# Kernel tuning notes

Measured on AMD Instinct MI355X. Metric: run time of the kernel, lower is better.

The kernel has to match this reference:

```python
import jax, jax.numpy as jnp
import numpy as np

EPS = 1e-7            # keras.backend.epsilon()
NEG = -1e30           # log-space 'zero' (avoid -inf for NaN-free grads)
SUB_SAMPLE = (2, 2)   # encoder conv subsampling factors (non-tensor forward arg)


def setup_inputs() -> dict:
    key = jax.random.key(0)
    k1, k2, k3, k4 = jax.random.split(key, 4)
    B, T, C, L = 128, 2000, 128, 200
    logits = jax.random.normal(k1, (B, T, C), jnp.float32)
    y_pred = jax.nn.softmax(logits, axis=-1)  # ctc_batch_cost expects probabilities
    labels = jax.random.randint(k2, (B, L), 0, C - 1, jnp.int32)  # never the blank (C-1)
    # raw frame counts; after two /2 subsamplings -> in [1000, 2000] <= T
    feat_lens = jax.random.randint(k3, (B,), 4000, 8000, jnp.int32)
    label_lens = jax.random.randint(k4, (B,), 50, L + 1, jnp.int32)
    return {"y_pred": y_pred, "labels": labels, "feat_lens": feat_lens, "label_lens": label_lens}


def _ctc_batch_cost(y_pred, labels, feat_lens, label_lens):
    """Faithful reimplementation of keras.backend.ctc_batch_cost (blank = C-1),
    with the CTCLayer's subsampling of feat_lens applied first."""
    for sub in SUB_SAMPLE:
        if sub > 1:
            feat_lens = (feat_lens + 1) // sub
    log_probs = jnp.log(y_pred + EPS)                 # [B,T,C]
    B, T, C = y_pred.shape
    L = labels.shape[1]
    S = 2 * L + 1
    blank = C - 1

    # extended label sequence: blank, l1, blank, l2, ..., blank  -> [B,S]
    ext = jnp.full((B, S), blank, jnp.int32).at[:, 1::2].set(labels)
    # skip transition s-2 -> s allowed iff ext[s] != blank and ext[s] != ext[s-2]
    skip_ok = jnp.concatenate(
        [jnp.zeros((B, 2), bool), (ext[:, 2:] != blank) & (ext[:, 2:] != ext[:, :-2])],
        axis=1,
    )
    bidx = jnp.arange(B)
    i1 = 2 * label_lens - 1   # last non-blank state
    i2 = 2 * label_lens       # trailing blank state

    lp = jnp.swapaxes(log_probs, 0, 1)                # [T,B,C], scan over time

    emit0 = jnp.take_along_axis(lp[0], ext, axis=1)   # [B,S]
    alpha0 = (jnp.full((B, S), NEG, jnp.float32)
              .at[:, 0].set(emit0[:, 0])
              .at[:, 1].set(emit0[:, 1]))
    ll0 = jnp.logaddexp(alpha0[bidx, i1], alpha0[bidx, i2])
    final0 = jnp.where(feat_lens == 1, ll0, NEG)

    def step(carry, inp):
        alpha, final = carry
        t, lp_t = inp
        emit = jnp.take_along_axis(lp_t, ext, axis=1)              # [B,S]
        a1 = jnp.pad(alpha, ((0, 0), (1, 0)), constant_values=NEG)[:, :-1]
        a2 = jnp.pad(alpha, ((0, 0), (2, 0)), constant_values=NEG)[:, :-2]
        m = jnp.logaddexp(alpha, a1)
        m = jnp.where(skip_ok, jnp.logaddexp(m, a2), m)
        alpha = m + emit
        ll = jnp.logaddexp(alpha[bidx, i1], alpha[bidx, i2])
        final = jnp.where(t == feat_lens - 1, ll, final)           # capture at last valid frame
        return (alpha, final), None

    (_, final), _ = jax.lax.scan(step, (alpha0, final0), (jnp.arange(1, T), lp[1:]))
    return -final[:, None]                                          # [B,1] like ctc_batch_cost


def reference(y_pred, labels, feat_lens, label_lens):
    return _ctc_batch_cost(y_pred, labels, feat_lens, label_lens)
```

## Files before the change

kernel.cpp:

```cpp
#include <hip/hip_runtime.h>
#include <math.h>

#define EPSQ 1e-7f
#define TDIM 2000
#define CDIM 128
#define LDIM 200
#define SPL  7
#define SENTE (-(1 << 30))

#define RING  0
#define LABSI 16384
#define PRODF 16584
#define CONSF 16585
#define SMEMN 16592


__device__ __forceinline__ float dpp_shr_f(float x) {
    return __int_as_float(__builtin_amdgcn_update_dpp(0, __float_as_int(x), 0x138, 0xf, 0xf, true));
}
__device__ __forceinline__ int dpp_shr_i(int x) {
    return __builtin_amdgcn_update_dpp(0, x, 0x138, 0xf, 0xf, true);
}
__device__ __forceinline__ float dpp_shl_f(float x) {
    return __int_as_float(__builtin_amdgcn_update_dpp(0, __float_as_int(x), 0x130, 0xf, 0xf, true));
}
__device__ __forceinline__ int dpp_shl_i(int x) {
    return __builtin_amdgcn_update_dpp(0, x, 0x130, 0xf, 0xf, true);
}

__device__ __forceinline__ void renorm_alpha(float a[SPL], int& E, float& fprev, int lane) {
    float mx = fmaxf(fmaxf(fmaxf(a[0], a[1]), fmaxf(a[2], a[3])),
                     fmaxf(fmaxf(a[4], a[5]), a[6]));
    bool zero = (mx == 0.f);
    int e = ((__float_as_int(mx) >> 23) & 0xff) - 127;
    int S_self = zero ? SENTE : (E + e);
    int S1 = dpp_shr_i(S_self);
    if (lane == 0) S1 = SENTE;
    int S2 = dpp_shr_i(S1);
    if (lane == 0) S2 = SENTE;
    int E_new = max(S_self, S1);
    int E_prevnew = max(S1, S2);
    int dg = E - E_new;
    float g = (zero || dg < -126) ? 0.f : __int_as_float((dg + 127) << 23);
#pragma unroll
    for (int j = 0; j < SPL; ++j) a[j] *= g;
    E = E_new;
    int df = E_prevnew - E_new;
    bool fz = (E_prevnew <= SENTE / 2) || (df < -126);
    if (df > 126) df = 126;
    fprev = fz ? 0.f : __int_as_float((df + 127) << 23);
}

__device__ __forceinline__ void renorm_beta(float b[SPL], int& E, float& fnext, int lane) {
    float mx = fmaxf(fmaxf(fmaxf(b[0], b[1]), fmaxf(b[2], b[3])),
                     fmaxf(fmaxf(b[4], b[5]), b[6]));
    bool zero = (mx == 0.f);
    int e = ((__float_as_int(mx) >> 23) & 0xff) - 127;
    int S_self = zero ? SENTE : (E + e);
    int S1 = dpp_shl_i(S_self);
    if (lane == 63) S1 = SENTE;
    int S2 = dpp_shl_i(S1);
    if (lane == 63) S2 = SENTE;
    int E_new = max(S_self, S1);
    int E_nextnew = max(S1, S2);
    int dg = E - E_new;
    float g = (zero || dg < -126) ? 0.f : __int_as_float((dg + 127) << 23);
#pragma unroll
    for (int j = 0; j < SPL; ++j) b[j] *= g;
    E = E_new;
    int df = E_nextnew - E_new;
    bool fz = (E_nextnew <= SENTE / 2) || (df < -126);
    if (df > 126) df = 126;
    fnext = fz ? 0.f : __int_as_float((df + 127) << 23);
}

#define A_STEP(TOFF) do {                                                     \
    float p6 = dpp_shr_f(a[6]) * fprev;                                       \
    float p5 = dpp_shr_f(a[5]) * fprev;                                       \
    float n0 = fmaf(skipf[0], p5,   a[0] + p6)   * q[(1+(TOFF))&3][0];        \
    float n1 = fmaf(skipf[1], p6,   a[1] + a[0]) * q[(1+(TOFF))&3][1];        \
    float n2 = fmaf(skipf[2], a[0], a[2] + a[1]) * q[(1+(TOFF))&3][2];        \
    float n3 = fmaf(skipf[3], a[1], a[3] + a[2]) * q[(1+(TOFF))&3][3];        \
    float n4 = fmaf(skipf[4], a[2], a[4] + a[3]) * q[(1+(TOFF))&3][4];        \
    float n5 = fmaf(skipf[5], a[3], a[5] + a[4]) * q[(1+(TOFF))&3][5];        \
    float n6 = fmaf(skipf[6], a[4], a[6] + a[5]) * q[(1+(TOFF))&3][6];        \
    a[0]=n0; a[1]=n1; a[2]=n2; a[3]=n3; a[4]=n4; a[5]=n5; a[6]=n6;            \
    if (t + (TOFF) == m) {                                                    \
        _Pragma("unroll")                                                     \
        for (int j = 0; j < SPL; ++j) ac[j] = a[j];                           \
        Eac = E;                                                              \
    }                                                                         \
    {   const int rr = ((t + (TOFF) + 3) & 127) << 7;                         \
        _Pragma("unroll")                                                     \
        for (int j = 0; j < SPL; ++j)                                         \
            q[(TOFF)&3][j] = ring[rr + cls[j]];                               \
    }                                                                         \
} while (0);

#define B_STEP(SOFF) do {                                                     \
    float c0 = bb[0]*q[(SOFF)&3][0], c1 = bb[1]*q[(SOFF)&3][1];               \
    float c2 = bb[2]*q[(SOFF)&3][2], c3 = bb[3]*q[(SOFF)&3][3];               \
    float c4 = bb[4]*q[(SOFF)&3][4], c5 = bb[5]*q[(SOFF)&3][5];               \
    float c6 = bb[6]*q[(SOFF)&3][6];                                          \
    float cn0 = dpp_shl_f(c0) * fnext;                                        \
    float cn1 = dpp_shl_f(c1) * fnext;                                        \
    bb[0] = fmaf(skb[0], c2, c0 + c1);                                        \
    bb[1] = fmaf(skb[1], c3, c1 + c2);                                        \
    bb[2] = fmaf(skb[2], c4, c2 + c3);                                        \
    bb[3] = fmaf(skb[3], c5, c3 + c4);                                        \
    bb[4] = fmaf(skb[4], c6, c4 + c5);                                        \
    bb[5] = fmaf(skb[5], cn0, c5 + c6);                                       \
    bb[6] = fmaf(skb[6], cn1, c6 + cn0);                                      \
    if (s + (SOFF) == scap) {                                                 \
        _Pragma("unroll")                                                     \
        for (int j = 0; j < SPL; ++j) bc[j] = bb[j];                          \
        Ebc = E;                                                              \
    }                                                                         \
    {   const int rr = ((t0 - s - (SOFF) - 3) & 127) << 7;                    \
        _Pragma("unroll")                                                     \
        for (int j = 0; j < SPL; ++j)                                         \
            q[(3+(SOFF))&3][j] = ring[rr + cls[j]];                           \
    }                                                                         \
} while (0);

#define LOADG(W, G) do {                                                      \
    _Pragma("unroll")                                                         \
    for (int i_ = 0; i_ < 8; ++i_) {                                          \
        int ii_ = (G) * 8 + i_; if (ii_ > iend) ii_ = iend;                   \
        int pr_ = role ? (pbase - ii_) : ii_;                                 \
        W[i_] = rp4[pr_ * 64 + lane];                                         \
    }                                                                         \
} while (0)

#define STOREG(W, G) do {                                                     \
    _Pragma("unroll")                                                         \
    for (int i_ = 0; i_ < 8; ++i_) {                                          \
        int ii_ = (G) * 8 + i_; if (ii_ > iend) ii_ = iend;                   \
        int pr_ = role ? (pbase - ii_) : ii_;                                 \
        float4 x_ = W[i_];                                                    \
        x_.x += EPSQ; x_.y += EPSQ; x_.z += EPSQ; x_.w += EPSQ;               \
        *(float4*)&smf[RING + (pr_ & 63) * 256 + lane * 4] = x_;              \
    }                                                                         \
} while (0)

__global__ void __launch_bounds__(128, 1)
__attribute__((amdgpu_waves_per_eu(1, 1)))
ctc_kernel(const float* __restrict__ y_pred,
           const int* __restrict__ labels,
           const int* __restrict__ feat_lens,
           const int* __restrict__ label_lens,
           float* __restrict__ ws)
{
    __shared__ int smem[SMEMN];
    float* smf = (float*)smem;
    volatile int* vsm = (volatile int*)smem;

    const int bid = blockIdx.x;
    const int b = bid >> 1;
    const int role = bid & 1;
    const int tid = threadIdx.x;
    const int lane = tid & 63;
    const int wv = tid >> 6;

    int f = feat_lens[b];
    f = (f + 1) >> 1; f = (f + 1) >> 1;
    const int Tbm1 = f - 1;
    const int m = f >> 1;

    if (tid < 2) smem[PRODF + tid] = 0;
    const int* labrow = labels + b * LDIM;
    for (int i = tid; i < LDIM; i += 128) smem[LABSI + i] = labrow[i];
    __syncthreads();

    const float4* rp4 = (const float4*)(y_pred + (size_t)b * TDIM * CDIM);

    if (wv == 1) {
        int iend, pbase;
        if (role == 0) { iend = (m + 18) >> 1; pbase = 0; }
        else {
            const int pstart = Tbm1 >> 1;
            int pl = (m - 18) >> 1; if (pl < 0) pl = 0;
            iend = pstart - pl; pbase = pstart;
        }
        const int ng = (iend >> 3) + 1;
        float4 w0[8], w1[8];
        LOADG(w0, 0);
        if (ng > 1) LOADG(w1, 1);
        int g = 0;
        while (true) {
            while (vsm[CONSF] + 64 < 8 * (g + 1)) __builtin_amdgcn_s_sleep(2);
            asm volatile("" ::: "memory");
            STOREG(w0, g);
            asm volatile("s_waitcnt lgkmcnt(0)" ::: "memory");
            vsm[PRODF] = 8 * (g + 1);
            if (g + 2 < ng) LOADG(w0, g + 2);
            ++g; if (g >= ng) break;
            while (vsm[CONSF] + 64 < 8 * (g + 1)) __builtin_amdgcn_s_sleep(2);
            asm volatile("" ::: "memory");
            STOREG(w1, g);
            asm volatile("s_waitcnt lgkmcnt(0)" ::: "memory");
            vsm[PRODF] = 8 * (g + 1);
            if (g + 2 < ng) LOADG(w1, g + 2);
            ++g; if (g >= ng) break;
        }
        return;
    }

    const int llen = label_lens[b];
    const int i1 = 2 * llen - 1, i2 = 2 * llen;
    int cls[SPL]; float skipf[SPL];
    const int s0 = lane * SPL;
#pragma unroll
    for (int j = 0; j < SPL; ++j) {
        int s = s0 + j;
        int c = CDIM - 1; float sk = 0.f;
        if (s < (2 * LDIM + 1) && (s & 1)) {
            int kk = s >> 1;
            c = smem[LABSI + kk];
            if (kk >= 1 && smem[LABSI + kk] != smem[LABSI + kk - 1]) sk = 1.f;
        }
        cls[j] = c; skipf[j] = sk;
    }
    const float* ring = &smf[RING];

    if (role == 0) {
        float a[SPL], q[4][SPL], ac[SPL];
        int E = 0, Eac = 0;
        float fprev = 0.f;
#pragma unroll
        for (int j = 0; j < SPL; ++j) { a[j] = 0.f; ac[j] = 0.f; }

        while (vsm[PRODF] < 2) __builtin_amdgcn_s_sleep(1);
        asm volatile("" ::: "memory");
#pragma unroll
        for (int j = 0; j < SPL; ++j) {
            q[0][j] = ring[(0 << 7) + cls[j]];
            q[1][j] = ring[(1 << 7) + cls[j]];
            q[2][j] = ring[(2 << 7) + cls[j]];
            q[3][j] = ring[(3 << 7) + cls[j]];
        }
        if (lane == 0) { a[0] = q[0][0]; a[1] = q[0][1]; }

        int t = 1;
        while (t <= m) {
            vsm[CONSF] = (t >= 2) ? (((t - 2) >> 1) + 1) : 0;
            int need = ((t + 18) >> 1) + 1;
            while (vsm[PRODF] < need) __builtin_amdgcn_s_sleep(1);
            asm volatile("" ::: "memory");
            renorm_alpha(a, E, fprev, lane);
            A_STEP(0) A_STEP(1) A_STEP(2) A_STEP(3)
            renorm_alpha(a, E, fprev, lane);
            A_STEP(4) A_STEP(5) A_STEP(6) A_STEP(7)
            renorm_alpha(a, E, fprev, lane);
            A_STEP(8) A_STEP(9) A_STEP(10) A_STEP(11)
            renorm_alpha(a, E, fprev, lane);
            A_STEP(12) A_STEP(13) A_STEP(14) A_STEP(15)
            t += 16;
        }
        vsm[CONSF] = 1 << 28;
        asm volatile("" ::: "memory");
        float* wsb = ws + (size_t)b * 1024;
#pragma unroll
        for (int j = 0; j < SPL; ++j) wsb[lane * SPL + j] = ac[j];
        ((int*)wsb)[448 + lane] = Eac;
    } else {
        float bb[SPL], q[4][SPL], bc[SPL];
        int E = 0, Ebc = 0;
        float fnext = 0.f;
#pragma unroll
        for (int j = 0; j < SPL; ++j) {
            int s = s0 + j;
            bb[j] = (s == i1 || s == i2) ? 1.f : 0.f;
            bc[j] = 0.f;
        }
        float skb[SPL];
#pragma unroll
        for (int j = 0; j < 5; ++j) skb[j] = skipf[j + 2];
        skb[5] = (lane == 63) ? 0.f : __shfl_down(skipf[0], 1, 64);
        skb[6] = (lane == 63) ? 0.f : __shfl_down(skipf[1], 1, 64);

        const int t0 = Tbm1;
        const int nb = t0 - m;
        const int scap = nb - 1;
        const int pstart = t0 >> 1;

        while (vsm[PRODF] < 2) __builtin_amdgcn_s_sleep(1);
        asm volatile("" ::: "memory");
#pragma unroll
        for (int j = 0; j < SPL; ++j) {
            q[0][j] = ring[((t0 & 127) << 7) + cls[j]];
            q[1][j] = ring[(((t0 - 1) & 127) << 7) + cls[j]];
            q[2][j] = ring[(((t0 - 2) & 127) << 7) + cls[j]];
            q[3][j] = 0.f;
        }

        int s = 0;
        while (s < nb) {
            int tcur = t0 - s;
            vsm[CONSF] = pstart - ((tcur + 2) >> 1) + 1;
            int need = pstart - ((tcur - 18) >> 1) + 1;
            while (vsm[PRODF] < need) __builtin_amdgcn_s_sleep(1);
            asm volatile("" ::: "memory");
            renorm_beta(bb, E, fnext, lane);
            B_STEP(0) B_STEP(1) B_STEP(2) B_STEP(3)
            renorm_beta(bb, E, fnext, lane);
            B_STEP(4) B_STEP(5) B_STEP(6) B_STEP(7)
            renorm_beta(bb, E, fnext, lane);
            B_STEP(8) B_STEP(9) B_STEP(10) B_STEP(11)
            renorm_beta(bb, E, fnext, lane);
            B_STEP(12) B_STEP(13) B_STEP(14) B_STEP(15)
            s += 16;
        }
        vsm[CONSF] = 1 << 28;
        asm volatile("" ::: "memory");
        float* wsb = ws + (size_t)b * 1024 + 512;
#pragma unroll
        for (int j = 0; j < SPL; ++j) wsb[lane * SPL + j] = bc[j];
        ((int*)wsb)[448 + lane] = Ebc;
    }
}

__global__ void __launch_bounds__(64, 1)
ctc_combine(const float* __restrict__ ws, float* __restrict__ out)
{
    const int b = blockIdx.x;
    const int lane = threadIdx.x & 63;
    const float* wa = ws + (size_t)b * 1024;
    const float* wb = wa + 512;
    const int Ea = ((const int*)wa)[448 + lane];
    const int Eb = ((const int*)wb)[448 + lane];
    float dot = 0.f;
#pragma unroll
    for (int j = 0; j < SPL; ++j)
        dot = fmaf(wa[lane * SPL + j], wb[lane * SPL + j], dot);
    float l2 = (dot > 0.f) ? (log2f(dot) + (float)(Ea + Eb)) : -1e30f;
    float M = l2;
#pragma unroll
    for (int d = 1; d < 64; d <<= 1) M = fmaxf(M, __shfl_xor(M, d, 64));
    float S = exp2f(l2 - M);
#pragma unroll
    for (int d = 1; d < 64; d <<= 1) S += __shfl_xor(S, d, 64);
    if (lane == 0) out[b] = -(M + log2f(S)) * 0.69314718055994530942f;
}

extern "C" void kernel_launch(void* const* d_in, const int* in_sizes, int n_in,
                              void* d_out, int out_size, void* d_ws, size_t ws_size,
                              hipStream_t stream) {
    (void)n_in; (void)out_size; (void)ws_size;
    const float* y_pred     = (const float*)d_in[0];
    const int*   labels     = (const int*)d_in[1];
    const int*   feat_lens  = (const int*)d_in[2];
    const int*   label_lens = (const int*)d_in[3];
    float* out = (float*)d_out;
    float* ws  = (float*)d_ws;
    const int B = in_sizes[2];
    ctc_kernel<<<B * 2, 128, 0, stream>>>(y_pred, labels, feat_lens, label_lens, ws);
    ctc_combine<<<B, 64, 0, stream>>>(ws, out);
}
```

Measured before the change: 271.5 us.

## Halve LDS ring, remap beta layout, unroll 64-step fast path with compile-time offsets

Shrinks the shared-memory ring from 128 to 64 frames and changes the producer store layout so the beta role writes frames in consumption order. The alpha and beta consumers get a 64-step fully unrolled main loop whose LDS read offsets are compile-time constants and which drops the per-step capture check. Producer/consumer handshakes happen every 32 steps instead of 16. This cuts per-step address arithmetic and branching, but the smaller ring reduces producer lead and adds code size and register pressure.

```diff
diff --git a/kernel.cpp b/kernel.cpp
--- a/kernel.cpp
+++ b/kernel.cpp
@@ -9,10 +9,10 @@
 #define SENTE (-(1 << 30))
 
 #define RING  0
-#define LABSI 16384
-#define PRODF 16584
-#define CONSF 16585
-#define SMEMN 16592
+#define LABSI 8192
+#define PRODF 8392
+#define CONSF 8393
+#define SMEMN 8400
 
 
 __device__ __forceinline__ float dpp_shr_f(float x) {
@@ -74,7 +74,23 @@
     fnext = fz ? 0.f : __int_as_float((df + 127) << 23);
 }
 
-#define A_STEP(TOFF) do {                                                     \
+#define A_STEPF(TOFF) do {                                                    \
+    float p6 = dpp_shr_f(a[6]) * fprev;                                       \
+    float p5 = dpp_shr_f(a[5]) * fprev;                                       \
+    float n0 = fmaf(skipf[0], p5,   a[0] + p6)   * q[(1+(TOFF))&3][0];        \
+    float n1 = fmaf(skipf[1], p6,   a[1] + a[0]) * q[(1+(TOFF))&3][1];        \
+    float n2 = fmaf(skipf[2], a[0], a[2] + a[1]) * q[(1+(TOFF))&3][2];        \
+    float n3 = fmaf(skipf[3], a[1], a[3] + a[2]) * q[(1+(TOFF))&3][3];        \
+    float n4 = fmaf(skipf[4], a[2], a[4] + a[3]) * q[(1+(TOFF))&3][4];        \
+    float n5 = fmaf(skipf[5], a[3], a[5] + a[4]) * q[(1+(TOFF))&3][5];        \
+    float n6 = fmaf(skipf[6], a[4], a[6] + a[5]) * q[(1+(TOFF))&3][6];        \
+    a[0]=n0; a[1]=n1; a[2]=n2; a[3]=n3; a[4]=n4; a[5]=n5; a[6]=n6;            \
+    _Pragma("unroll")                                                         \
+    for (int j = 0; j < SPL; ++j)                                             \
+        q[(TOFF)&3][j] = ring[((((TOFF)+4)&63)<<7) + cls[j]];                 \
+} while (0);
+
+#define A_TAIL(TOFF) do {                                                     \
     float p6 = dpp_shr_f(a[6]) * fprev;                                       \
     float p5 = dpp_shr_f(a[5]) * fprev;                                       \
     float n0 = fmaf(skipf[0], p5,   a[0] + p6)   * q[(1+(TOFF))&3][0];        \
@@ -90,14 +106,33 @@
         for (int j = 0; j < SPL; ++j) ac[j] = a[j];                           \
         Eac = E;                                                              \
     }                                                                         \
-    {   const int rr = ((t + (TOFF) + 3) & 127) << 7;                         \
+    {   const int rr = ((t + (TOFF) + 3) & 63) << 7;                          \
         _Pragma("unroll")                                                     \
         for (int j = 0; j < SPL; ++j)                                         \
             q[(TOFF)&3][j] = ring[rr + cls[j]];                               \
     }                                                                         \
 } while (0);
 
-#define B_STEP(SOFF) do {                                                     \
+#define B_STEPF(SOFF) do {                                                    \
+    float c0 = bb[0]*q[(SOFF)&3][0], c1 = bb[1]*q[(SOFF)&3][1];               \
+    float c2 = bb[2]*q[(SOFF)&3][2], c3 = bb[3]*q[(SOFF)&3][3];               \
+    float c4 = bb[4]*q[(SOFF)&3][4], c5 = bb[5]*q[(SOFF)&3][5];               \
+    float c6 = bb[6]*q[(SOFF)&3][6];                                          \
+    float cn0 = dpp_shl_f(c0) * fnext;                                        \
+    float cn1 = dpp_shl_f(c1) * fnext;                                        \
+    bb[0] = fmaf(skb[0], c2, c0 + c1);                                        \
+    bb[1] = fmaf(skb[1], c3, c1 + c2);                                        \
+    bb[2] = fmaf(skb[2], c4, c2 + c3);                                        \
+    bb[3] = fmaf(skb[3], c5, c3 + c4);                                        \
+    bb[4] = fmaf(skb[4], c6, c4 + c5);                                        \
+    bb[5] = fmaf(skb[5], cn0, c5 + c6);                                       \
+    bb[6] = fmaf(skb[6], cn1, c6 + cn0);                                      \
+    _Pragma("unroll")                                                         \
+    for (int j = 0; j < SPL; ++j)                                             \
+        q[(3+(SOFF))&3][j] = ring[((((SOFF)+3)&63)<<7) + cls[j]];             \
+} while (0);
+
+#define B_TAIL(SOFF) do {                                                     \
     float c0 = bb[0]*q[(SOFF)&3][0], c1 = bb[1]*q[(SOFF)&3][1];               \
     float c2 = bb[2]*q[(SOFF)&3][2], c3 = bb[3]*q[(SOFF)&3][3];               \
     float c4 = bb[4]*q[(SOFF)&3][4], c5 = bb[5]*q[(SOFF)&3][5];               \
@@ -116,12 +151,17 @@
         for (int j = 0; j < SPL; ++j) bc[j] = bb[j];                          \
         Ebc = E;                                                              \
     }                                                                         \
-    {   const int rr = ((t0 - s - (SOFF) - 3) & 127) << 7;                    \
+    {   const int rr = ((s + (SOFF) + 3) & 63) << 7;                          \
         _Pragma("unroll")                                                     \
         for (int j = 0; j < SPL; ++j)                                         \
             q[(3+(SOFF))&3][j] = ring[rr + cls[j]];                           \
     }                                                                         \
 } while (0);
+
+#define ABLK(T) renorm_alpha(a, E, fprev, lane); \
+    A_STEPF(T) A_STEPF((T)+1) A_STEPF((T)+2) A_STEPF((T)+3)
+#define BBLK(T) renorm_beta(bb, E, fnext, lane); \
+    B_STEPF(T) B_STEPF((T)+1) B_STEPF((T)+2) B_STEPF((T)+3)
 
 #define LOADG(W, G) do {                                                      \
     _Pragma("unroll")                                                         \
@@ -139,7 +179,11 @@
         int pr_ = role ? (pbase - ii_) : ii_;                                 \
         float4 x_ = W[i_];                                                    \
         x_.x += EPSQ; x_.y += EPSQ; x_.z += EPSQ; x_.w += EPSQ;               \
-        *(float4*)&smf[RING + (pr_ & 63) * 256 + lane * 4] = x_;              \
+        int fa_;                                                              \
+        if (role) { int jj_ = (Tbm1 - 2 * pr_) - (lane >> 5);                 \
+                    fa_ = ((jj_ & 63) << 7) + ((lane & 31) << 2); }           \
+        else      { fa_ = ((pr_ & 31) << 8) + (lane << 2); }                  \
+        *(float4*)&smf[RING + fa_] = x_;                                      \
     }                                                                         \
 } while (0)
 
@@ -188,14 +232,14 @@
         if (ng > 1) LOADG(w1, 1);
         int g = 0;
         while (true) {
-            while (vsm[CONSF] + 64 < 8 * (g + 1)) __builtin_amdgcn_s_sleep(2);
+            while (vsm[CONSF] + 32 < 8 * (g + 1)) __builtin_amdgcn_s_sleep(2);
             asm volatile("" ::: "memory");
             STOREG(w0, g);
             asm volatile("s_waitcnt lgkmcnt(0)" ::: "memory");
             vsm[PRODF] = 8 * (g + 1);
             if (g + 2 < ng) LOADG(w0, g + 2);
             ++g; if (g >= ng) break;
-            while (vsm[CONSF] + 64 < 8 * (g + 1)) __builtin_amdgcn_s_sleep(2);
+            while (vsm[CONSF] + 32 < 8 * (g + 1)) __builtin_amdgcn_s_sleep(2);
             asm volatile("" ::: "memory");
             STOREG(w1, g);
             asm volatile("s_waitcnt lgkmcnt(0)" ::: "memory");
@@ -242,19 +286,39 @@
         if (lane == 0) { a[0] = q[0][0]; a[1] = q[0][1]; }
 
         int t = 1;
+        while (t + 64 <= m) {
+            vsm[CONSF] = (t >= 2) ? (((t - 2) >> 1) + 1) : 0;
+            {
+                int need = ((t + 34) >> 1) + 1;
+                while (vsm[PRODF] < need) __builtin_amdgcn_s_sleep(1);
+                asm volatile("" ::: "memory");
+            }
+            ABLK(0) ABLK(4) ABLK(8) ABLK(12)
+            ABLK(16) ABLK(20) ABLK(24) ABLK(28)
+            {
+                int tc = t + 32;
+                vsm[CONSF] = ((tc - 2) >> 1) + 1;
+                int need = ((tc + 34) >> 1) + 1;
+                while (vsm[PRODF] < need) __builtin_amdgcn_s_sleep(1);
+                asm volatile("" ::: "memory");
+            }
+            ABLK(32) ABLK(36) ABLK(40) ABLK(44)
+            ABLK(48) ABLK(52) ABLK(56) ABLK(60)
+            t += 64;
+        }
         while (t <= m) {
             vsm[CONSF] = (t >= 2) ? (((t - 2) >> 1) + 1) : 0;
             int need = ((t + 18) >> 1) + 1;
             while (vsm[PRODF] < need) __builtin_amdgcn_s_sleep(1);
             asm volatile("" ::: "memory");
             renorm_alpha(a, E, fprev, lane);
-            A_STEP(0) A_STEP(1) A_STEP(2) A_STEP(3)
+            A_TAIL(0) A_TAIL(1) A_TAIL(2) A_TAIL(3)
             renorm_alpha(a, E, fprev, lane);
-            A_STEP(4) A_STEP(5) A_STEP(6) A_STEP(7)
+            A_TAIL(4) A_TAIL(5) A_TAIL(6) A_TAIL(7)
             renorm_alpha(a, E, fprev, lane);
-            A_STEP(8) A_STEP(9) A_STEP(10) A_STEP(11)
+            A_TAIL(8) A_TAIL(9) A_TAIL(10) A_TAIL(11)
             renorm_alpha(a, E, fprev, lane);
-            A_STEP(12) A_STEP(13) A_STEP(14) A_STEP(15)
+            A_TAIL(12) A_TAIL(13) A_TAIL(14) A_TAIL(15)
             t += 16;
         }
         vsm[CONSF] = 1 << 28;
@@ -288,13 +352,34 @@
         asm volatile("" ::: "memory");
 #pragma unroll
         for (int j = 0; j < SPL; ++j) {
-            q[0][j] = ring[((t0 & 127) << 7) + cls[j]];
-            q[1][j] = ring[(((t0 - 1) & 127) << 7) + cls[j]];
-            q[2][j] = ring[(((t0 - 2) & 127) << 7) + cls[j]];
+            q[0][j] = ring[(0 << 7) + cls[j]];
+            q[1][j] = ring[(1 << 7) + cls[j]];
+            q[2][j] = ring[(2 << 7) + cls[j]];
             q[3][j] = 0.f;
         }
 
         int s = 0;
+        while (s + 64 <= scap) {
+            {
+                int tcur = t0 - s;
+                vsm[CONSF] = pstart - ((tcur + 2) >> 1) + 1;
+                int need = pstart - ((tcur - 34) >> 1) + 1;
+                while (vsm[PRODF] < need) __builtin_amdgcn_s_sleep(1);
+                asm volatile("" ::: "memory");
+            }
+            BBLK(0) BBLK(4) BBLK(8) BBLK(12)
+            BBLK(16) BBLK(20) BBLK(24) BBLK(28)
+            {
+                int tcur = t0 - s - 32;
+                vsm[CONSF] = pstart - ((tcur + 2) >> 1) + 1;
+                int need = pstart - ((tcur - 34) >> 1) + 1;
+                while (vsm[PRODF] < need) __builtin_amdgcn_s_sleep(1);
+                asm volatile("" ::: "memory");
+            }
+            BBLK(32) BBLK(36) BBLK(40) BBLK(44)
+            BBLK(48) BBLK(52) BBLK(56) BBLK(60)
+            s += 64;
+        }
         while (s < nb) {
             int tcur = t0 - s;
             vsm[CONSF] = pstart - ((tcur + 2) >> 1) + 1;
@@ -302,13 +387,13 @@
             while (vsm[PRODF] < need) __builtin_amdgcn_s_sleep(1);
             asm volatile("" ::: "memory");
             renorm_beta(bb, E, fnext, lane);
-            B_STEP(0) B_STEP(1) B_STEP(2) B_STEP(3)
+            B_TAIL(0) B_TAIL(1) B_TAIL(2) B_TAIL(3)
             renorm_beta(bb, E, fnext, lane);
-            B_STEP(4) B_STEP(5) B_STEP(6) B_STEP(7)
+            B_TAIL(4) B_TAIL(5) B_TAIL(6) B_TAIL(7)
             renorm_beta(bb, E, fnext, lane);
-            B_STEP(8) B_STEP(9) B_STEP(10) B_STEP(11)
+            B_TAIL(8) B_TAIL(9) B_TAIL(10) B_TAIL(11)
             renorm_beta(bb, E, fnext, lane);
-            B_STEP(12) B_STEP(13) B_STEP(14) B_STEP(15)
+            B_TAIL(12) B_TAIL(13) B_TAIL(14) B_TAIL(15)
             s += 16;
         }
         vsm[CONSF] = 1 << 28;
```

After: 250.4 us. 7.8% less time.

## Fold producer wave into compute wave with register double-buffered prefetch

Applied to the files above, without the earlier changes.

Removes the separate producer wavefront and its shared-memory flag handshaking (spin-waits with sleep). Each compute wave now issues its own global loads into two register buffers and writes them into a smaller 64-row LDS ring between unrolled step blocks. The state layout moves from 7 to 8 states per lane, so blank/label states alternate at fixed positions, the blank probability is loaded once per step, and the skip multiplies on blank states disappear. The cost is much higher register pressure and global-load latency that is no longer hidden by a separate wave.

```diff
diff --git a/kernel.cpp b/kernel.cpp
--- a/kernel.cpp
+++ b/kernel.cpp
@@ -5,15 +5,11 @@
 #define TDIM 2000
 #define CDIM 128
 #define LDIM 200
-#define SPL  7
+#define SPL  8
 #define SENTE (-(1 << 30))
 
-#define RING  0
-#define LABSI 16384
-#define PRODF 16584
-#define CONSF 16585
-#define SMEMN 16592
-
+#define LABSI 8192
+#define SMEMN 8400
 
 __device__ __forceinline__ float dpp_shr_f(float x) {
     return __int_as_float(__builtin_amdgcn_update_dpp(0, __float_as_int(x), 0x138, 0xf, 0xf, true));
@@ -30,7 +26,7 @@
 
 __device__ __forceinline__ void renorm_alpha(float a[SPL], int& E, float& fprev, int lane) {
     float mx = fmaxf(fmaxf(fmaxf(a[0], a[1]), fmaxf(a[2], a[3])),
-                     fmaxf(fmaxf(a[4], a[5]), a[6]));
+                     fmaxf(fmaxf(a[4], a[5]), fmaxf(a[6], a[7])));
     bool zero = (mx == 0.f);
     int e = ((__float_as_int(mx) >> 23) & 0xff) - 127;
     int S_self = zero ? SENTE : (E + e);
@@ -53,7 +49,7 @@
 
 __device__ __forceinline__ void renorm_beta(float b[SPL], int& E, float& fnext, int lane) {
     float mx = fmaxf(fmaxf(fmaxf(b[0], b[1]), fmaxf(b[2], b[3])),
-                     fmaxf(fmaxf(b[4], b[5]), b[6]));
+                     fmaxf(fmaxf(b[4], b[5]), fmaxf(b[6], b[7])));
     bool zero = (mx == 0.f);
     int e = ((__float_as_int(mx) >> 23) & 0xff) - 127;
     int S_self = zero ? SENTE : (E + e);
@@ -74,77 +70,138 @@
     fnext = fz ? 0.f : __int_as_float((df + 127) << 23);
 }
 
-#define A_STEP(TOFF) do {                                                     \
-    float p6 = dpp_shr_f(a[6]) * fprev;                                       \
-    float p5 = dpp_shr_f(a[5]) * fprev;                                       \
-    float n0 = fmaf(skipf[0], p5,   a[0] + p6)   * q[(1+(TOFF))&3][0];        \
-    float n1 = fmaf(skipf[1], p6,   a[1] + a[0]) * q[(1+(TOFF))&3][1];        \
-    float n2 = fmaf(skipf[2], a[0], a[2] + a[1]) * q[(1+(TOFF))&3][2];        \
-    float n3 = fmaf(skipf[3], a[1], a[3] + a[2]) * q[(1+(TOFF))&3][3];        \
-    float n4 = fmaf(skipf[4], a[2], a[4] + a[3]) * q[(1+(TOFF))&3][4];        \
-    float n5 = fmaf(skipf[5], a[3], a[5] + a[4]) * q[(1+(TOFF))&3][5];        \
-    float n6 = fmaf(skipf[6], a[4], a[6] + a[5]) * q[(1+(TOFF))&3][6];        \
-    a[0]=n0; a[1]=n1; a[2]=n2; a[3]=n3; a[4]=n4; a[5]=n5; a[6]=n6;            \
-    if (t + (TOFF) == m) {                                                    \
+#define RA renorm_alpha(a, E, fprev, lane);
+#define RB renorm_beta(bb, E, fnext, lane);
+
+#define A_STEPF(CT) do {                                                      \
+    const int cs_ = (1+(CT))&3;                                               \
+    float p7 = dpp_shr_f(a[7]) * fprev;                                       \
+    float n0 = (a[0] + p7) * qb[cs_];                                         \
+    float n1 = fmaf(sk1, p7, a[1] + a[0]) * ql[cs_][0];                       \
+    float n2 = (a[2] + a[1]) * qb[cs_];                                       \
+    float n3 = fmaf(sk3, a[1], a[3] + a[2]) * ql[cs_][1];                     \
+    float n4 = (a[4] + a[3]) * qb[cs_];                                       \
+    float n5 = fmaf(sk5, a[3], a[5] + a[4]) * ql[cs_][2];                     \
+    float n6 = (a[6] + a[5]) * qb[cs_];                                       \
+    float n7 = fmaf(sk7, a[5], a[7] + a[6]) * ql[cs_][3];                     \
+    a[0]=n0;a[1]=n1;a[2]=n2;a[3]=n3;a[4]=n4;a[5]=n5;a[6]=n6;a[7]=n7;          \
+    { const int ro_ = (((CT)+4)&63)<<7;                                       \
+      qb[(CT)&3]    = ringF[ro_ + 127];                                       \
+      ql[(CT)&3][0] = ringF[ro_ + cl0];                                       \
+      ql[(CT)&3][1] = ringF[ro_ + cl1];                                       \
+      ql[(CT)&3][2] = ringF[ro_ + cl2];                                       \
+      ql[(CT)&3][3] = ringF[ro_ + cl3]; }                                     \
+} while (0);
+
+#define A_TAIL(CT) do {                                                       \
+    const int cs_ = (1+(CT))&3;                                               \
+    float p7 = dpp_shr_f(a[7]) * fprev;                                       \
+    float n0 = (a[0] + p7) * qb[cs_];                                         \
+    float n1 = fmaf(sk1, p7, a[1] + a[0]) * ql[cs_][0];                       \
+    float n2 = (a[2] + a[1]) * qb[cs_];                                       \
+    float n3 = fmaf(sk3, a[1], a[3] + a[2]) * ql[cs_][1];                     \
+    float n4 = (a[4] + a[3]) * qb[cs_];                                       \
+    float n5 = fmaf(sk5, a[3], a[5] + a[4]) * ql[cs_][2];                     \
+    float n6 = (a[6] + a[5]) * qb[cs_];                                       \
+    float n7 = fmaf(sk7, a[5], a[7] + a[6]) * ql[cs_][3];                     \
+    a[0]=n0;a[1]=n1;a[2]=n2;a[3]=n3;a[4]=n4;a[5]=n5;a[6]=n6;a[7]=n7;          \
+    if (t + (CT) == m) {                                                      \
         _Pragma("unroll")                                                     \
         for (int j = 0; j < SPL; ++j) ac[j] = a[j];                           \
         Eac = E;                                                              \
     }                                                                         \
-    {   const int rr = ((t + (TOFF) + 3) & 127) << 7;                         \
-        _Pragma("unroll")                                                     \
-        for (int j = 0; j < SPL; ++j)                                         \
-            q[(TOFF)&3][j] = ring[rr + cls[j]];                               \
-    }                                                                         \
+    { const int ro_ = ((t+(CT)+3)&63)<<7;                                     \
+      qb[(CT)&3]    = ringF[ro_ + 127];                                       \
+      ql[(CT)&3][0] = ringF[ro_ + cl0];                                       \
+      ql[(CT)&3][1] = ringF[ro_ + cl1];                                       \
+      ql[(CT)&3][2] = ringF[ro_ + cl2];                                       \
+      ql[(CT)&3][3] = ringF[ro_ + cl3]; }                                     \
 } while (0);
 
-#define B_STEP(SOFF) do {                                                     \
-    float c0 = bb[0]*q[(SOFF)&3][0], c1 = bb[1]*q[(SOFF)&3][1];               \
-    float c2 = bb[2]*q[(SOFF)&3][2], c3 = bb[3]*q[(SOFF)&3][3];               \
-    float c4 = bb[4]*q[(SOFF)&3][4], c5 = bb[5]*q[(SOFF)&3][5];               \
-    float c6 = bb[6]*q[(SOFF)&3][6];                                          \
+#define B_STEPF(CT) do {                                                      \
+    const int cs_ = (CT)&3;                                                   \
+    float c0 = bb[0]*qb[cs_],    c1 = bb[1]*ql[cs_][0];                       \
+    float c2 = bb[2]*qb[cs_],    c3 = bb[3]*ql[cs_][1];                       \
+    float c4 = bb[4]*qb[cs_],    c5 = bb[5]*ql[cs_][2];                       \
+    float c6 = bb[6]*qb[cs_],    c7 = bb[7]*ql[cs_][3];                       \
     float cn0 = dpp_shl_f(c0) * fnext;                                        \
     float cn1 = dpp_shl_f(c1) * fnext;                                        \
-    bb[0] = fmaf(skb[0], c2, c0 + c1);                                        \
-    bb[1] = fmaf(skb[1], c3, c1 + c2);                                        \
-    bb[2] = fmaf(skb[2], c4, c2 + c3);                                        \
-    bb[3] = fmaf(skb[3], c5, c3 + c4);                                        \
-    bb[4] = fmaf(skb[4], c6, c4 + c5);                                        \
-    bb[5] = fmaf(skb[5], cn0, c5 + c6);                                       \
-    bb[6] = fmaf(skb[6], cn1, c6 + cn0);                                      \
-    if (s + (SOFF) == scap) {                                                 \
+    bb[0] = c0 + c1;                                                          \
+    bb[1] = fmaf(sk3, c3, c1 + c2);                                           \
+    bb[2] = c2 + c3;                                                          \
+    bb[3] = fmaf(sk5, c5, c3 + c4);                                           \
+    bb[4] = c4 + c5;                                                          \
+    bb[5] = fmaf(sk7, c7, c5 + c6);                                           \
+    bb[6] = c6 + c7;                                                          \
+    bb[7] = fmaf(skb7, cn1, c7 + cn0);                                        \
+    { const int ro_ = (((CT)+3)&63)<<7;                                       \
+      qb[(3+(CT))&3]    = ringF[ro_ + 127];                                   \
+      ql[(3+(CT))&3][0] = ringF[ro_ + cl0];                                   \
+      ql[(3+(CT))&3][1] = ringF[ro_ + cl1];                                   \
+      ql[(3+(CT))&3][2] = ringF[ro_ + cl2];                                   \
+      ql[(3+(CT))&3][3] = ringF[ro_ + cl3]; }                                 \
+} while (0);
+
+#define B_TAIL(CT) do {                                                       \
+    const int cs_ = (CT)&3;                                                   \
+    float c0 = bb[0]*qb[cs_],    c1 = bb[1]*ql[cs_][0];                       \
+    float c2 = bb[2]*qb[cs_],    c3 = bb[3]*ql[cs_][1];                       \
+    float c4 = bb[4]*qb[cs_],    c5 = bb[5]*ql[cs_][2];                       \
+    float c6 = bb[6]*qb[cs_],    c7 = bb[7]*ql[cs_][3];                       \
+    float cn0 = dpp_shl_f(c0) * fnext;                                        \
+    float cn1 = dpp_shl_f(c1) * fnext;                                        \
+    bb[0] = c0 + c1;                                                          \
+    bb[1] = fmaf(sk3, c3, c1 + c2);                                           \
+    bb[2] = c2 + c3;                                                          \
+    bb[3] = fmaf(sk5, c5, c3 + c4);                                           \
+    bb[4] = c4 + c5;                                                          \
+    bb[5] = fmaf(sk7, c7, c5 + c6);                                           \
+    bb[6] = c6 + c7;                                                          \
+    bb[7] = fmaf(skb7, cn1, c7 + cn0);                                        \
+    if (s + (CT) == scap) {                                                   \
         _Pragma("unroll")                                                     \
         for (int j = 0; j < SPL; ++j) bc[j] = bb[j];                          \
         Ebc = E;                                                              \
     }                                                                         \
-    {   const int rr = ((t0 - s - (SOFF) - 3) & 127) << 7;                    \
-        _Pragma("unroll")                                                     \
-        for (int j = 0; j < SPL; ++j)                                         \
-            q[(3+(SOFF))&3][j] = ring[rr + cls[j]];                           \
-    }                                                                         \
+    { const int ro_ = ((s+(CT)+3)&63)<<7;                                     \
+      qb[(3+(CT))&3]    = ringF[ro_ + 127];                                   \
+      ql[(3+(CT))&3][0] = ringF[ro_ + cl0];                                   \
+      ql[(3+(CT))&3][1] = ringF[ro_ + cl1];                                   \
+      ql[(3+(CT))&3][2] = ringF[ro_ + cl2];                                   \
+      ql[(3+(CT))&3][3] = ringF[ro_ + cl3]; }                                 \
 } while (0);
 
-#define LOADG(W, G) do {                                                      \
-    _Pragma("unroll")                                                         \
-    for (int i_ = 0; i_ < 8; ++i_) {                                          \
-        int ii_ = (G) * 8 + i_; if (ii_ > iend) ii_ = iend;                   \
-        int pr_ = role ? (pbase - ii_) : ii_;                                 \
-        W[i_] = rp4[pr_ * 64 + lane];                                         \
-    }                                                                         \
-} while (0)
-
-#define STOREG(W, G) do {                                                     \
-    _Pragma("unroll")                                                         \
-    for (int i_ = 0; i_ < 8; ++i_) {                                          \
-        int ii_ = (G) * 8 + i_; if (ii_ > iend) ii_ = iend;                   \
-        int pr_ = role ? (pbase - ii_) : ii_;                                 \
+#define A4(T)  A_STEPF(T) A_STEPF((T)+1) A_STEPF((T)+2) A_STEPF((T)+3)
+#define A16(T) RA A4(T) RA A4((T)+4) RA A4((T)+8) RA A4((T)+12)
+#define AT4(T) A_TAIL(T) A_TAIL((T)+1) A_TAIL((T)+2) A_TAIL((T)+3)
+#define B4(T)  B_STEPF(T) B_STEPF((T)+1) B_STEPF((T)+2) B_STEPF((T)+3)
+#define B16(T) RB B4(T) RB B4((T)+4) RB B4((T)+8) RB B4((T)+12)
+#define BT4(T) B_TAIL(T) B_TAIL((T)+1) B_TAIL((T)+2) B_TAIL((T)+3)
+
+#define A_LOAD(W, KC) do { const int b_ = 8*(KC);                             \
+    _Pragma("unroll") for (int i_ = 0; i_ < 8; ++i_) {                        \
+        int pi_ = b_ + i_; if (pi_ > pend) pi_ = pend;                        \
+        W[i_] = rp4[(size_t)pi_*64 + lane]; } } while(0)
+#define A_WRITE(W, KC) do { const int b_ = 8*(KC);                            \
+    _Pragma("unroll") for (int i_ = 0; i_ < 8; ++i_) {                        \
+        int pi_ = b_ + i_; if (pi_ > pend) pi_ = pend;                        \
         float4 x_ = W[i_];                                                    \
         x_.x += EPSQ; x_.y += EPSQ; x_.z += EPSQ; x_.w += EPSQ;               \
-        *(float4*)&smf[RING + (pr_ & 63) * 256 + lane * 4] = x_;              \
-    }                                                                         \
-} while (0)
-
-__global__ void __launch_bounds__(128, 1)
-__attribute__((amdgpu_waves_per_eu(1, 1)))
+        *(float4*)&ringF[(((2*pi_)&63)<<7) + (lane<<2)] = x_; } } while(0)
+
+#define B_LOAD(W, KC) do { const int b_ = 8*(KC);                             \
+    _Pragma("unroll") for (int i_ = 0; i_ < 8; ++i_) {                        \
+        int ii_ = b_ + i_; if (ii_ > pstart) ii_ = pstart;                    \
+        W[i_] = rp4[(size_t)(pstart - ii_)*64 + lane]; } } while(0)
+#define B_WRITE(W, KC) do { const int b_ = 8*(KC);                            \
+    _Pragma("unroll") for (int i_ = 0; i_ < 8; ++i_) {                        \
+        int ii_ = b_ + i_; if (ii_ > pstart) ii_ = pstart;                    \
+        int jj_ = t0 - 2*(pstart - ii_) - hi_;                                \
+        float4 x_ = W[i_];                                                    \
+        x_.x += EPSQ; x_.y += EPSQ; x_.z += EPSQ; x_.w += EPSQ;               \
+        *(float4*)&ringF[((jj_&63)<<7) + lo16_] = x_; } } while(0)
+
+__global__ void __launch_bounds__(64, 1)
 ctc_kernel(const float* __restrict__ y_pred,
            const int* __restrict__ labels,
            const int* __restrict__ feat_lens,
@@ -152,171 +209,131 @@
            float* __restrict__ ws)
 {
     __shared__ int smem[SMEMN];
-    float* smf = (float*)smem;
-    volatile int* vsm = (volatile int*)smem;
+    float* ringF = (float*)smem;
 
     const int bid = blockIdx.x;
     const int b = bid >> 1;
     const int role = bid & 1;
-    const int tid = threadIdx.x;
-    const int lane = tid & 63;
-    const int wv = tid >> 6;
+    const int lane = threadIdx.x & 63;
 
     int f = feat_lens[b];
     f = (f + 1) >> 1; f = (f + 1) >> 1;
     const int Tbm1 = f - 1;
     const int m = f >> 1;
 
-    if (tid < 2) smem[PRODF + tid] = 0;
     const int* labrow = labels + b * LDIM;
-    for (int i = tid; i < LDIM; i += 128) smem[LABSI + i] = labrow[i];
+    for (int i = lane; i < LDIM; i += 64) smem[LABSI + i] = labrow[i];
     __syncthreads();
 
-    const float4* rp4 = (const float4*)(y_pred + (size_t)b * TDIM * CDIM);
-
-    if (wv == 1) {
-        int iend, pbase;
-        if (role == 0) { iend = (m + 18) >> 1; pbase = 0; }
-        else {
-            const int pstart = Tbm1 >> 1;
-            int pl = (m - 18) >> 1; if (pl < 0) pl = 0;
-            iend = pstart - pl; pbase = pstart;
-        }
-        const int ng = (iend >> 3) + 1;
-        float4 w0[8], w1[8];
-        LOADG(w0, 0);
-        if (ng > 1) LOADG(w1, 1);
-        int g = 0;
-        while (true) {
-            while (vsm[CONSF] + 64 < 8 * (g + 1)) __builtin_amdgcn_s_sleep(2);
-            asm volatile("" ::: "memory");
-            STOREG(w0, g);
-            asm volatile("s_waitcnt lgkmcnt(0)" ::: "memory");
-            vsm[PRODF] = 8 * (g + 1);
-            if (g + 2 < ng) LOADG(w0, g + 2);
-            ++g; if (g >= ng) break;
-            while (vsm[CONSF] + 64 < 8 * (g + 1)) __builtin_amdgcn_s_sleep(2);
-            asm volatile("" ::: "memory");
-            STOREG(w1, g);
-            asm volatile("s_waitcnt lgkmcnt(0)" ::: "memory");
-            vsm[PRODF] = 8 * (g + 1);
-            if (g + 2 < ng) LOADG(w1, g + 2);
-            ++g; if (g >= ng) break;
-        }
-        return;
-    }
-
-    const int llen = label_lens[b];
-    const int i1 = 2 * llen - 1, i2 = 2 * llen;
-    int cls[SPL]; float skipf[SPL];
-    const int s0 = lane * SPL;
-#pragma unroll
-    for (int j = 0; j < SPL; ++j) {
-        int s = s0 + j;
+    int cl[4]; float skl[4];
+#pragma unroll
+    for (int u = 0; u < 4; ++u) {
+        int kk = 4*lane + u;
         int c = CDIM - 1; float sk = 0.f;
-        if (s < (2 * LDIM + 1) && (s & 1)) {
-            int kk = s >> 1;
+        if (kk < LDIM && (8*lane + 2*u + 1) < (2*LDIM + 1)) {
             c = smem[LABSI + kk];
             if (kk >= 1 && smem[LABSI + kk] != smem[LABSI + kk - 1]) sk = 1.f;
         }
-        cls[j] = c; skipf[j] = sk;
+        cl[u] = c; skl[u] = sk;
     }
-    const float* ring = &smf[RING];
+    const float sk1 = skl[0], sk3 = skl[1], sk5 = skl[2], sk7 = skl[3];
+    const int cl0 = cl[0], cl1 = cl[1], cl2 = cl[2], cl3 = cl[3];
+
+    const float4* rp4 = (const float4*)(y_pred + (size_t)b * TDIM * CDIM);
+    const int llen = label_lens[b];
+    const int i1 = 2*llen - 1, i2 = 2*llen;
+    const int s0 = lane * SPL;
 
     if (role == 0) {
-        float a[SPL], q[4][SPL], ac[SPL];
-        int E = 0, Eac = 0;
-        float fprev = 0.f;
+        const int pend = (m + 18) >> 1;
+        float4 wA[8], wB[8];
+        float a[SPL], ac[SPL];
+        float qb[4], ql[4][4];
+        int E = 0, Eac = 0; float fprev = 0.f;
 #pragma unroll
         for (int j = 0; j < SPL; ++j) { a[j] = 0.f; ac[j] = 0.f; }
-
-        while (vsm[PRODF] < 2) __builtin_amdgcn_s_sleep(1);
-        asm volatile("" ::: "memory");
-#pragma unroll
-        for (int j = 0; j < SPL; ++j) {
-            q[0][j] = ring[(0 << 7) + cls[j]];
-            q[1][j] = ring[(1 << 7) + cls[j]];
-            q[2][j] = ring[(2 << 7) + cls[j]];
-            q[3][j] = ring[(3 << 7) + cls[j]];
-        }
-        if (lane == 0) { a[0] = q[0][0]; a[1] = q[0][1]; }
-
-        int t = 1;
+        qb[0] = 0.f; ql[0][0]=ql[0][1]=ql[0][2]=ql[0][3]=0.f;
+
+        A_LOAD(wA, 0); A_LOAD(wB, 1); A_WRITE(wA, 0);
+        asm volatile("s_waitcnt lgkmcnt(0)" ::: "memory");
+#pragma unroll
+        for (int r = 1; r <= 3; ++r) {
+            qb[r]    = ringF[(r<<7) + 127];
+            ql[r][0] = ringF[(r<<7) + cl0];
+            ql[r][1] = ringF[(r<<7) + cl1];
+            ql[r][2] = ringF[(r<<7) + cl2];
+            ql[r][3] = ringF[(r<<7) + cl3];
+        }
+        { float v0b = ringF[127], v0l = ringF[cl0];
+          if (lane == 0) { a[0] = v0b; a[1] = v0l; } }
+
+        int t = 1, k = 0;
+        while (t + 64 <= m) {
+            A_LOAD(wA, k+2); A_WRITE(wB, k+1); A16(0)
+            A_LOAD(wB, k+3); A_WRITE(wA, k+2); A16(16)
+            A_LOAD(wA, k+4); A_WRITE(wB, k+3); A16(32)
+            A_LOAD(wB, k+5); A_WRITE(wA, k+4); A16(48)
+            t += 64; k += 4;
+        }
         while (t <= m) {
-            vsm[CONSF] = (t >= 2) ? (((t - 2) >> 1) + 1) : 0;
-            int need = ((t + 18) >> 1) + 1;
-            while (vsm[PRODF] < need) __builtin_amdgcn_s_sleep(1);
-            asm volatile("" ::: "memory");
-            renorm_alpha(a, E, fprev, lane);
-            A_STEP(0) A_STEP(1) A_STEP(2) A_STEP(3)
-            renorm_alpha(a, E, fprev, lane);
-            A_STEP(4) A_STEP(5) A_STEP(6) A_STEP(7)
-            renorm_alpha(a, E, fprev, lane);
-            A_STEP(8) A_STEP(9) A_STEP(10) A_STEP(11)
-            renorm_alpha(a, E, fprev, lane);
-            A_STEP(12) A_STEP(13) A_STEP(14) A_STEP(15)
-            t += 16;
-        }
-        vsm[CONSF] = 1 << 28;
-        asm volatile("" ::: "memory");
-        float* wsb = ws + (size_t)b * 1024;
+            if (k & 1) { A_LOAD(wB, k+2); A_WRITE(wA, k+1); }
+            else       { A_LOAD(wA, k+2); A_WRITE(wB, k+1); }
+            RA AT4(0) RA AT4(4) RA AT4(8) RA AT4(12)
+            t += 16; k += 1;
+        }
+        float* wsb = ws + (size_t)b * 2048;
 #pragma unroll
         for (int j = 0; j < SPL; ++j) wsb[lane * SPL + j] = ac[j];
-        ((int*)wsb)[448 + lane] = Eac;
+        ((int*)wsb)[512 + lane] = Eac;
     } else {
-        float bb[SPL], q[4][SPL], bc[SPL];
-        int E = 0, Ebc = 0;
-        float fnext = 0.f;
+        const int t0 = Tbm1;
+        const int nb = t0 - m;
+        const int scap = nb - 1;
+        const int pstart = t0 >> 1;
+        const int hi_ = lane >> 5;
+        const int lo16_ = (lane & 31) << 2;
+        float4 wA[8], wB[8];
+        float bb[SPL], bc[SPL];
+        float qb[4], ql[4][4];
+        int E = 0, Ebc = 0; float fnext = 0.f;
 #pragma unroll
         for (int j = 0; j < SPL; ++j) {
             int s = s0 + j;
             bb[j] = (s == i1 || s == i2) ? 1.f : 0.f;
             bc[j] = 0.f;
         }
-        float skb[SPL];
-#pragma unroll
-        for (int j = 0; j < 5; ++j) skb[j] = skipf[j + 2];
-        skb[5] = (lane == 63) ? 0.f : __shfl_down(skipf[0], 1, 64);
-        skb[6] = (lane == 63) ? 0.f : __shfl_down(skipf[1], 1, 64);
-
-        const int t0 = Tbm1;
-        const int nb = t0 - m;
-        const int scap = nb - 1;
-        const int pstart = t0 >> 1;
-
-        while (vsm[PRODF] < 2) __builtin_amdgcn_s_sleep(1);
-        asm volatile("" ::: "memory");
-#pragma unroll
-        for (int j = 0; j < SPL; ++j) {
-            q[0][j] = ring[((t0 & 127) << 7) + cls[j]];
-            q[1][j] = ring[(((t0 - 1) & 127) << 7) + cls[j]];
-            q[2][j] = ring[(((t0 - 2) & 127) << 7) + cls[j]];
-            q[3][j] = 0.f;
-        }
-
-        int s = 0;
+        const float skb7 = (lane == 63) ? 0.f : __shfl_down(sk1, 1, 64);
+        qb[3] = 0.f; ql[3][0]=ql[3][1]=ql[3][2]=ql[3][3]=0.f;
+
+        B_LOAD(wA, 0); B_LOAD(wB, 1); B_WRITE(wA, 0);
+        asm volatile("s_waitcnt lgkmcnt(0)" ::: "memory");
+#pragma unroll
+        for (int r = 0; r <= 2; ++r) {
+            qb[r]    = ringF[(r<<7) + 127];
+            ql[r][0] = ringF[(r<<7) + cl0];
+            ql[r][1] = ringF[(r<<7) + cl1];
+            ql[r][2] = ringF[(r<<7) + cl2];
+            ql[r][3] = ringF[(r<<7) + cl3];
+        }
+
+        int s = 0, k = 0;
+        while (s + 64 <= scap) {
+            B_LOAD(wA, k+2); B_WRITE(wB, k+1); B16(0)
+            B_LOAD(wB, k+3); B_WRITE(wA, k+2); B16(16)
+            B_LOAD(wA, k+4); B_WRITE(wB, k+3); B16(32)
+            B_LOAD(wB, k+5); B_WRITE(wA, k+4); B16(48)
+            s += 64; k += 4;
+        }
         while (s < nb) {
-            int tcur = t0 - s;
-            vsm[CONSF] = pstart - ((tcur + 2) >> 1) + 1;
-            int need = pstart - ((tcur - 18) >> 1) + 1;
-            while (vsm[PRODF] < need) __builtin_amdgcn_s_sleep(1);
-            asm volatile("" ::: "memory");
-            renorm_beta(bb, E, fnext, lane);
-            B_STEP(0) B_STEP(1) B_STEP(2) B_STEP(3)
-            renorm_beta(bb, E, fnext, lane);
-            B_STEP(4) B_STEP(5) B_STEP(6) B_STEP(7)
-            renorm_beta(bb, E, fnext, lane);
-            B_STEP(8) B_STEP(9) B_STEP(10) B_STEP(11)
-            renorm_beta(bb, E, fnext, lane);
-            B_STEP(12) B_STEP(13) B_STEP(14) B_STEP(15)
-            s += 16;
-        }
-        vsm[CONSF] = 1 << 28;
-        asm volatile("" ::: "memory");
-        float* wsb = ws + (size_t)b * 1024 + 512;
+            if (k & 1) { B_LOAD(wB, k+2); B_WRITE(wA, k+1); }
+            else       { B_LOAD(wA, k+2); B_WRITE(wB, k+1); }
+            RB BT4(0) RB BT4(4) RB BT4(8) RB BT4(12)
+            s += 16; k += 1;
+        }
+        float* wsb = ws + (size_t)b * 2048 + 1024;
 #pragma unroll
         for (int j = 0; j < SPL; ++j) wsb[lane * SPL + j] = bc[j];
-        ((int*)wsb)[448 + lane] = Ebc;
+        ((int*)wsb)[512 + lane] = Ebc;
     }
 }
 
@@ -325,10 +342,10 @@
 {
     const int b = blockIdx.x;
     const int lane = threadIdx.x & 63;
-    const float* wa = ws + (size_t)b * 1024;
-    const float* wb = wa + 512;
-    const int Ea = ((const int*)wa)[448 + lane];
-    const int Eb = ((const int*)wb)[448 + lane];
+    const float* wa = ws + (size_t)b * 2048;
+    const float* wb = wa + 1024;
+    const int Ea = ((const int*)wa)[512 + lane];
+    const int Eb = ((const int*)wb)[512 + lane];
     float dot = 0.f;
 #pragma unroll
     for (int j = 0; j < SPL; ++j)
@@ -354,6 +371,6 @@
     float* out = (float*)d_out;
     float* ws  = (float*)d_ws;
     const int B = in_sizes[2];
-    ctc_kernel<<<B * 2, 128, 0, stream>>>(y_pred, labels, feat_lens, label_lens, ws);
+    ctc_kernel<<<B * 2, 64, 0, stream>>>(y_pred, labels, feat_lens, label_lens, ws);
     ctc_combine<<<B, 64, 0, stream>>>(ws, out);
 }
```

After: 265.5 us. 1.02x faster.
